# Kernel tuning notes

Measured on AMD Instinct MI355X. Metric: run time of the kernel, lower is better.

The kernel has to match this reference:

```python
import jax, jax.numpy as jnp
import numpy as np

B, N, C = 8, 6000, 21            # batch, proposals (pre_nms_topn), total_labels
VARIANCES = jnp.array([0.1, 0.1, 0.2, 0.2], jnp.float32)
MAX_TOTAL = 200                   # max_total_size == max_output_size_per_class
SCORE_THR = 0.5
IOU_THR = 0.5                     # tf combined_non_max_suppression default
NEG = -1e9                        # finite sentinel for suppressed scores


def setup_inputs() -> dict:
    key = jax.random.key(0)
    k1, k2, k3, k4 = jax.random.split(key, 4)
    # valid normalized rois: y1,x1 in [0,0.8), positive height/width
    yx1 = jax.random.uniform(k1, (B, N, 2), jnp.float32) * 0.8
    hw = jax.random.uniform(k4, (B, N, 2), jnp.float32) * 0.2 + 0.01
    roi_bboxes = jnp.concatenate([yx1, yx1 + hw], axis=-1)  # [B,N,4] y1x1y2x2
    pred_deltas = jax.random.normal(k2, (B, N, C * 4), jnp.float32) * 0.5
    pred_label_probs = jax.random.uniform(k3, (B, N, C), jnp.float32)
    return {"roi_bboxes": roi_bboxes, "pred_deltas": pred_deltas,
            "pred_label_probs": pred_label_probs}


def reference(roi_bboxes, pred_deltas, pred_label_probs):
    # --- bbox delta decoding ---
    deltas = pred_deltas.reshape(B, N, C, 4) * VARIANCES          # [B,N,C,4]
    roi = roi_bboxes[:, :, None, :]                               # [B,N,1,4]
    anc_h = roi[..., 2] - roi[..., 0]
    anc_w = roi[..., 3] - roi[..., 1]
    anc_cy = roi[..., 0] + 0.5 * anc_h
    anc_cx = roi[..., 1] + 0.5 * anc_w
    bh = jnp.exp(deltas[..., 2]) * anc_h
    bw = jnp.exp(deltas[..., 3]) * anc_w
    bcy = deltas[..., 0] * anc_h + anc_cy
    bcx = deltas[..., 1] * anc_w + anc_cx
    y1 = bcy - 0.5 * bh
    x1 = bcx - 0.5 * bw
    y2 = y1 + bh
    x2 = x1 + bw
    boxes = jnp.stack([y1, x1, y2, x2], axis=-1)                  # [B,N,C,4]
    boxes = jnp.clip(boxes, 0.0, 1.0)  # combined NMS clip_boxes=True default

    # zero out scores where argmax class is background (0)
    lbl = jnp.argmax(pred_label_probs, axis=-1)                   # [B,N]
    scores = jnp.where((lbl != 0)[..., None], pred_label_probs, 0.0)

    boxes = boxes.transpose(0, 2, 1, 3)                           # [B,C,N,4]
    scores = scores.transpose(0, 2, 1)                            # [B,C,N]
    s0 = jnp.where(scores > SCORE_THR, scores, NEG)

    areas = (jnp.maximum(boxes[..., 2] - boxes[..., 0], 0.0) *
             jnp.maximum(boxes[..., 3] - boxes[..., 1], 0.0))     # [B,C,N]

    # --- greedy per-class NMS, vectorized over (B,C) ---
    def step(s, _):
        idx = jnp.argmax(s, axis=-1)                              # [B,C]
        val = jnp.take_along_axis(s, idx[..., None], axis=-1)[..., 0]
        box = jnp.take_along_axis(boxes, idx[..., None, None], axis=2)[..., 0, :]
        valid = val > NEG * 0.5
        iy1 = jnp.maximum(box[..., None, 0], boxes[..., 0])
        ix1 = jnp.maximum(box[..., None, 1], boxes[..., 1])
        iy2 = jnp.minimum(box[..., None, 2], boxes[..., 2])
        ix2 = jnp.minimum(box[..., None, 3], boxes[..., 3])
        inter = jnp.maximum(iy2 - iy1, 0.0) * jnp.maximum(ix2 - ix1, 0.0)
        sel_a = (jnp.maximum(box[..., 2] - box[..., 0], 0.0) *
                 jnp.maximum(box[..., 3] - box[..., 1], 0.0))
        iou = inter / (sel_a[..., None] + areas - inter + 1e-8)   # [B,C,N]
        s = jnp.where((iou > IOU_THR) & valid[..., None], NEG, s)
        return s, (box, val, valid)

    _, (sel_box, sel_val, sel_ok) = jax.lax.scan(step, s0, None, length=MAX_TOTAL)
    # [T,B,C,*] -> [B, C*T, *]
    sel_box = sel_box.transpose(1, 2, 0, 3).reshape(B, C * MAX_TOTAL, 4)
    sel_val = sel_val.transpose(1, 2, 0).reshape(B, C * MAX_TOTAL)
    sel_ok = sel_ok.transpose(1, 2, 0).reshape(B, C * MAX_TOTAL)
    cls = jnp.broadcast_to(jnp.arange(C, dtype=jnp.float32)[None, :, None],
                           (B, C, MAX_TOTAL)).reshape(B, C * MAX_TOTAL)

    sel_val = jnp.where(sel_ok, sel_val, NEG)
    top_s, top_i = jax.lax.top_k(sel_val, MAX_TOTAL)              # [B,200]
    fb = jnp.take_along_axis(sel_box, top_i[..., None], axis=1)
    fc = jnp.take_along_axis(cls, top_i, axis=1)
    ok = top_s > NEG * 0.5
    final_scores = jnp.where(ok, top_s, 0.0)
    final_bboxes = jnp.where(ok[..., None], fb, 0.0)
    final_labels = jnp.where(ok, fc, 0.0)
    return final_bboxes, final_labels, final_scores
```

## Files before the change

### kernel.cpp

```cpp
#include <hip/hip_runtime.h>

#define B_    8
#define N_    6000
#define C_    21
#define MAXT  200
#define NEGV  -1000000000.0f
#define UCAP  4096
#define CCAP  1024
#define CTGT  512
#define NBUCK 64
#define NTH   1024
#define NENT  (C_ * MAXT)
#define NBLK  (B_ * C_)


__device__ __forceinline__ unsigned ford(float f) {
  unsigned u = __float_as_uint(f);
  return (u & 0x80000000u) ? ~u : (u | 0x80000000u);
}
__device__ __forceinline__ float funord(unsigned o) {
  unsigned u = (o & 0x80000000u) ? (o ^ 0x80000000u) : ~o;
  return __uint_as_float(u);
}

__device__ __forceinline__ float4 decode_box(const float* __restrict__ roi,
                                             const float* __restrict__ deltas,
                                             int b, int n, int c)
{
#pragma clang fp contract(off)
  float4 r = *(const float4*)(roi + ((size_t)b * N_ + n) * 4);
  float4 d = *(const float4*)(deltas + ((size_t)b * N_ + n) * (C_ * 4) + c * 4);
  float d0 = d.x * 0.1f, d1 = d.y * 0.1f, d2 = d.z * 0.2f, d3 = d.w * 0.2f;
  float ah = r.z - r.x, aw = r.w - r.y;
  float acy = r.x + 0.5f * ah, acx = r.y + 0.5f * aw;
  float bh = expf(d2) * ah, bw = expf(d3) * aw;
  float bcy = d0 * ah + acy, bcx = d1 * aw + acx;
  float y1 = bcy - 0.5f * bh, x1 = bcx - 0.5f * bw;
  float y2 = y1 + bh, x2 = x1 + bw;
  y1 = fminf(fmaxf(y1, 0.f), 1.f); x1 = fminf(fmaxf(x1, 0.f), 1.f);
  y2 = fminf(fmaxf(y2, 0.f), 1.f); x2 = fminf(fmaxf(x2, 0.f), 1.f);
  return make_float4(y1, x1, y2, x2);
}

__device__ __forceinline__ float iou_ref(float4 s, float4 o) {
#pragma clang fp contract(off)
  float iy1 = fmaxf(s.x, o.x), ix1 = fmaxf(s.y, o.y);
  float iy2 = fminf(s.z, o.z), ix2 = fminf(s.w, o.w);
  float inter = fmaxf(iy2 - iy1, 0.f) * fmaxf(ix2 - ix1, 0.f);
  float sa = fmaxf(s.z - s.x, 0.f) * fmaxf(s.w - s.y, 0.f);
  float oa = fmaxf(o.z - o.x, 0.f) * fmaxf(o.w - o.y, 0.f);
  return inter / (sa + oa - inter + 1e-08f);
}

struct Smem {
  unsigned long long ukeys[UCAP];
  unsigned long long cbuf[CCAP];
  float4 cboxAll[512];
  float4 comm[MAXT];
  unsigned long long kill[64];
  unsigned long long s_dead[16];
  int hist[NBUCK];
  int ctr[NBUCK];
  int wcnt[16];
  int s_cnt, s_clen, s_ncomm, s_blo, s_len, s_m, s_mx;
};

__global__ __launch_bounds__(256) void prep_kernel(
    const float* __restrict__ probs, float* __restrict__ probsT)
{
  int t = blockIdx.x * 256 + threadIdx.x;
  if (t >= B_ * N_) return;
  int b = t / N_, n = t - b * N_;
  const float* pr = probs + (size_t)t * C_;
  float p[C_];
  #pragma unroll
  for (int k = 0; k < C_; ++k) p[k] = pr[k];
  float mx = p[0]; int am = 0;
  #pragma unroll
  for (int k = 1; k < C_; ++k) { if (p[k] > mx) { mx = p[k]; am = k; } }
  float msk = (am != 0) ? 1.0f : 0.0f;
  #pragma unroll
  for (int c = 0; c < C_; ++c)
    probsT[((size_t)b * C_ + c) * N_ + n] = p[c] * msk;
}

__global__ __launch_bounds__(NTH) void nms_kernel(
    const float* __restrict__ roi, const float* __restrict__ deltas,
    const float* __restrict__ probs, const float* __restrict__ probsT,
    float* __restrict__ sel_val, float* __restrict__ sel_box)
{
#pragma clang fp contract(off)
  __shared__ Smem sm;
  const int bc = blockIdx.x, b = bc / C_, c = bc % C_;
  const int tid = threadIdx.x, lane = tid & 63, wv = tid >> 6;

  if (tid < NBUCK) sm.hist[tid] = 0;
  if (tid == 0) { sm.s_cnt = 0; sm.s_ncomm = 0; }
  __syncthreads();

  int M;
  const float* rowT = probsT ? (probsT + (size_t)bc * N_) : nullptr;
  if (rowT) {
    float scv[6];
    #pragma unroll
    for (int it = 0; it < 6; ++it) {
      int n = it * NTH + tid;
      scv[it] = (n < N_) ? rowT[n] : 0.f;
    }
    int off[6];
    int wtot = 0;
    #pragma unroll
    for (int it = 0; it < 6; ++it) {
      bool cand = (scv[it] > 0.5f);
      unsigned long long m = __ballot(cand);
      off[it] = wtot + __popcll(m & ((1ULL << lane) - 1ULL));
      wtot += __popcll(m);
    }
    if (lane == 0) sm.wcnt[wv] = wtot;
    __syncthreads();
    int wbase = 0, mtot = 0;
    #pragma unroll
    for (int w = 0; w < 16; ++w) {
      int t2 = sm.wcnt[w];
      if (w < wv) wbase += t2;
      mtot += t2;
    }
    #pragma unroll
    for (int it = 0; it < 6; ++it) {
      if (scv[it] > 0.5f) {
        int pos = wbase + off[it];
        if (pos < UCAP) {
          unsigned hi = ford(scv[it]);
          int n = it * NTH + tid;
          sm.ukeys[pos] = ((unsigned long long)hi << 32) |
                          (unsigned)(0xFFFFFFFFu - (unsigned)n);
          atomicAdd(&sm.hist[(hi >> 17) & (NBUCK - 1)], 1);
        }
      }
    }
    __syncthreads();
    M = mtot < UCAP ? mtot : UCAP;
  } else {
    for (int base0 = 0; base0 < N_; base0 += NTH) {
      int n = base0 + tid;
      bool cand = false;
      float sc = 0.f;
      if (n < N_) {
        const float* pr = probs + ((size_t)b * N_ + n) * C_;
        float mx = pr[0]; int am = 0;
        #pragma unroll
        for (int k = 1; k < C_; ++k) { float v = pr[k]; if (v > mx) { mx = v; am = k; } }
        if (am != 0) sc = pr[c];
        cand = (sc > 0.5f);
      }
      unsigned long long m = __ballot(cand);
      int wcnt2 = __popcll(m);
      int bslot = 0;
      if (lane == 0 && wcnt2) bslot = atomicAdd(&sm.s_cnt, wcnt2);
      bslot = __shfl(bslot, 0);
      if (cand) {
        int pos = bslot + __popcll(m & ((1ULL << lane) - 1ULL));
        if (pos < UCAP) {
          unsigned hi = ford(sc);
          sm.ukeys[pos] = ((unsigned long long)hi << 32) |
                          (unsigned)(0xFFFFFFFFu - (unsigned)n);
          atomicAdd(&sm.hist[(hi >> 17) & (NBUCK - 1)], 1);
        }
      }
    }
    __syncthreads();
    M = sm.s_cnt < UCAP ? sm.s_cnt : UCAP;
  }

  float* sv = sel_val + (size_t)bc * MAXT;
  float* sb = sel_box + (size_t)bc * MAXT * 4;

  int bhi = NBUCK - 1;
  while (true) {
    if (sm.s_ncomm >= MAXT || bhi < 0) break;

    if (wv == 0) {
      int h = (lane <= bhi) ? sm.hist[bhi - lane] : 0;
      int p = h;
      #pragma unroll
      for (int d = 1; d < 64; d <<= 1) {
        int o = __shfl_up(p, d);
        if (lane >= d) p += o;
      }
      unsigned long long ok = __ballot(p <= CTGT);
      int m = __popcll(ok);
      if (m == 0) m = 1;
      if (m > bhi + 1) m = bhi + 1;
      int len = __shfl(p, m - 1);
      if (lane < m) sm.ctr[bhi - lane] = p - h;
      int hv = (lane < m) ? h : 0;
      #pragma unroll
      for (int d = 1; d < 64; d <<= 1) hv = max(hv, __shfl_xor(hv, d));
      if (lane == 0) {
        sm.s_blo = bhi - (m - 1); sm.s_len = len; sm.s_clen = 0;
        sm.s_m = m; sm.s_mx = hv;
      }
    }
    __syncthreads();
    int blo = sm.s_blo;
    if (sm.s_len == 0) break;
    int mbk = sm.s_m, mxb = sm.s_mx;

    for (int i = tid; i < M; i += NTH) {
      unsigned long long kk = sm.ukeys[i];
      int bk = (int)((kk >> 49) & (NBUCK - 1));
      if (bk >= blo && bk <= bhi) {
        int slot = atomicAdd(&sm.ctr[bk], 1);
        if (slot < CCAP) sm.cbuf[slot] = kk;
      }
    }
    __syncthreads();
    int alen = sm.s_len < CCAP ? sm.s_len : CCAP;

    if (alen > 0) {
      if (alen <= 512 && mxb <= 128) {
        for (int j = wv; j < mbk; j += 16) {
          int bk = bhi - j;
          int len = sm.hist[bk];
          if (len <= 0) continue;
          int base = sm.ctr[bk] - len;
          if (len <= 64) {
            unsigned long long v = (lane < len) ? sm.cbuf[base + lane] : 0ULL;
            #pragma unroll
            for (int k = 2; k <= 64; k <<= 1) {
              for (int jj = k >> 1; jj > 0; jj >>= 1) {
                unsigned long long w = __shfl_xor(v, jj);
                bool takeMax = ((lane & jj) == 0) == ((lane & k) == 0);
                if ((w > v) == takeMax) v = w;
              }
            }
            if (lane < len) sm.cbuf[base + lane] = v;
          } else {
            unsigned long long v0 = (lane < len) ? sm.cbuf[base + lane] : 0ULL;
            unsigned long long v1 = (64 + lane < len) ? sm.cbuf[base + 64 + lane] : 0ULL;
            #pragma unroll
            for (int k = 2; k <= 128; k <<= 1) {
              for (int jj = k >> 1; jj > 0; jj >>= 1) {
                if (jj == 64) {
                  unsigned long long a = (v0 > v1) ? v0 : v1;
                  unsigned long long bmin = (v0 > v1) ? v1 : v0;
                  v0 = a; v1 = bmin;
                } else {
                  unsigned long long w0 = __shfl_xor(v0, jj);
                  unsigned long long w1 = __shfl_xor(v1, jj);
                  bool e0k = ((lane & k) == 0);
                  bool e1k = (((lane + 64) & k) == 0);
                  bool jz = ((lane & jj) == 0);
                  bool tm0 = (jz == e0k);
                  bool tm1 = (jz == e1k);
                  if ((w0 > v0) == tm0) v0 = w0;
                  if ((w1 > v1) == tm1) v1 = w1;
                }
              }
            }
            if (lane < len) sm.cbuf[base + lane] = v0;
            if (64 + lane < len) sm.cbuf[base + 64 + lane] = v1;
          }
        }
        __syncthreads();
      } else {
        int SORTP = 64;
        while (SORTP < alen) SORTP <<= 1;
        unsigned long long v = (tid < alen) ? sm.cbuf[tid] : 0ULL;
        for (int k = 2; k <= SORTP; k <<= 1) {
          for (int j = k >> 1; j > 0; j >>= 1) {
            bool takeMax = ((tid & j) == 0) == ((tid & k) == 0);
            unsigned long long w;
            if (j >= 64) {
              __syncthreads(); if (tid < SORTP) sm.cbuf[tid] = v; __syncthreads();
              w = sm.cbuf[tid ^ j];
            } else {
              w = __shfl_xor(v, j);
            }
            if (tid < SORTP && (w > v) == takeMax) v = w;
          }
        }
        __syncthreads();
        if (tid < SORTP) sm.cbuf[tid] = v;
        __syncthreads();
      }

      if (tid < alen && tid < 512) {
        int n = (int)(0xFFFFFFFFu - (unsigned)(sm.cbuf[tid] & 0xFFFFFFFFull));
        sm.cboxAll[tid] = decode_box(roi, deltas, b, n, c);
      }
      __syncthreads();

      int start = 0;
      int wlen = alen < 512 ? alen : 512;
      while (true) {
        int nc = sm.s_ncomm;
        if (nc >= MAXT || start >= wlen) break;
        int bs = min(64, wlen - start);

        float4 ib = sm.cboxAll[start + lane];
        #pragma unroll
        for (int r = 0; r < 4; ++r) {
          int j = (wv << 2) | r;
          float4 jb4 = sm.cboxAll[start + j];
          bool kf = (j < bs) && (lane < bs) && (lane > j) &&
                    (iou_ref(jb4, ib) > 0.5f);
          unsigned long long rowm = __ballot(kf);
          if (lane == 0) sm.kill[j] = rowm;
        }
        {
          bool dead = false;
          if (lane < bs) {
            for (int jc = wv; jc < nc; jc += 16) {
              if (iou_ref(sm.comm[jc], ib) > 0.5f) { dead = true; break; }
            }
          }
          unsigned long long dm = __ballot(dead);
          if (lane == 0) sm.s_dead[wv] = dm;
        }
        __syncthreads();

        if (wv == 0) {
          unsigned long long sup = sm.s_dead[0];
          #pragma unroll
          for (int w2 = 1; w2 < 16; ++w2) sup |= sm.s_dead[w2];
          unsigned long long row = sm.kill[lane];
          #pragma unroll
          for (int s5 = 0; s5 < 6; ++s5) {
            const unsigned long long Ms[6] = {
              0x5555555555555555ULL, 0x3333333333333333ULL,
              0x0F0F0F0F0F0F0F0FULL, 0x00FF00FF00FF00FFULL,
              0x0000FFFF0000FFFFULL, 0x00000000FFFFFFFFULL };
            int d = 1 << s5;
            unsigned long long other = __shfl_xor(row, d);
            unsigned long long Mk = Ms[s5];
            row = ((lane & d) == 0) ? ((row & Mk) | ((other & Mk) << d))
                                    : ((row & ~Mk) | ((other & ~Mk) >> d));
          }
          unsigned long long col = row;

          unsigned long long alive = ~sup;
          if (bs < 64) alive &= (1ULL << bs) - 1ULL;
          unsigned long long pend = alive, chosen = 0ULL;
          while (pend) {
            bool rdy_b = ((col & pend) == 0ULL);
            unsigned long long rdy = __ballot(rdy_b) & pend;
            bool kld_b = ((col & chosen) != 0ULL);
            unsigned long long kl = __ballot(kld_b);
            chosen |= rdy & ~kl;
            pend &= ~rdy;
          }
          int take = MAXT - nc;
          if (__popcll(chosen) > take) {
            bool keep = ((chosen >> lane) & 1ULL) &&
                        (__popcll(chosen & ((1ULL << lane) - 1ULL)) < take);
            chosen = __ballot(keep);
          }
          if ((chosen >> lane) & 1ULL) {
            int rnk = nc + __popcll(chosen & ((1ULL << lane) - 1ULL));
            float4 bb2 = sm.cboxAll[start + lane];
            sm.comm[rnk] = bb2;
            sv[rnk] = funord((unsigned)(sm.cbuf[start + lane] >> 32));
            sb[(size_t)rnk * 4 + 0] = bb2.x; sb[(size_t)rnk * 4 + 1] = bb2.y;
            sb[(size_t)rnk * 4 + 2] = bb2.z; sb[(size_t)rnk * 4 + 3] = bb2.w;
          }
          if (lane == 0) sm.s_ncomm = nc + __popcll(chosen);
        }
        __syncthreads();
        start += bs;
      }
    }
    bhi = blo - 1;
  }

  int T = sm.s_ncomm;
  for (int j2 = T + tid; j2 < MAXT; j2 += NTH) sv[j2] = NEGV;
}

__global__ __launch_bounds__(NTH) void merge2_kernel(
    const float* __restrict__ sel_val, const float* __restrict__ sel_box,
    float* __restrict__ out)
{
  __shared__ Smem sm;
  const int bc = blockIdx.x;
  const int b = bc / C_, sc = bc % C_;
  const int tid = threadIdx.x;
  int* s_rank = reinterpret_cast<int*>(sm.cboxAll);

  for (int i = tid; i < NENT; i += NTH) {
    float v = sel_val[(size_t)b * NENT + i];
    unsigned long long key = ((unsigned long long)ford(v) << 32) |
                             (unsigned)(0xFFFFFFFFu - (unsigned)i);
    if (i < UCAP) sm.ukeys[i] = key; else sm.cbuf[i - UCAP] = key;
  }
  if (tid < MAXT) s_rank[tid] = 0;
  __syncthreads();

  auto klds = [&](int i) -> unsigned long long {
    return (i < UCAP) ? sm.ukeys[i] : sm.cbuf[i - UCAP];
  };

  if (tid < 1000) {
    int q = tid / MAXT, t = tid - q * MAXT;
    int e = sc * MAXT + t;
    unsigned long long mykey = klds(e);
    int part = 0;
    for (int cc = q; cc < C_; cc += 5) {
      int lo = 0, hi = MAXT;
      while (lo < hi) {
        int mid = (lo + hi) >> 1;
        if (klds(cc * MAXT + mid) > mykey) lo = mid + 1; else hi = mid;
      }
      part += lo;
    }
    atomicAdd(&s_rank[t], part);
  }
  __syncthreads();

  if (tid < MAXT) {
    int t = tid;
    int e = sc * MAXT + t;
    int rank = s_rank[t];
    if (rank < MAXT) {
      float* obx = out + (size_t)b * MAXT * 4;
      float* olb = out + (size_t)B_ * MAXT * 4 + (size_t)b * MAXT;
      float* osc = out + (size_t)B_ * MAXT * 5 + (size_t)b * MAXT;
      float v = funord((unsigned)(klds(e) >> 32));
      if (v > NEGV * 0.5f) {
        osc[rank] = v;
        olb[rank] = (float)sc;
        const float* bp = sel_box + ((size_t)b * NENT + e) * 4;
        obx[rank * 4 + 0] = bp[0]; obx[rank * 4 + 1] = bp[1];
        obx[rank * 4 + 2] = bp[2]; obx[rank * 4 + 3] = bp[3];
      } else {
        osc[rank] = 0.f; olb[rank] = 0.f;
        obx[rank * 4 + 0] = 0.f; obx[rank * 4 + 1] = 0.f;
        obx[rank * 4 + 2] = 0.f; obx[rank * 4 + 3] = 0.f;
      }
    }
  }
}

extern "C" void kernel_launch(void* const* d_in, const int* in_sizes, int n_in,
                              void* d_out, int out_size, void* d_ws, size_t ws_size,
                              hipStream_t stream)
{
  const float* roi    = (const float*)d_in[0];
  const float* deltas = (const float*)d_in[1];
  const float* probs  = (const float*)d_in[2];
  float* out = (float*)d_out;
  float* ws  = (float*)d_ws;

  float* sel_val = ws;
  float* sel_box = ws + (size_t)B_ * NENT;
  float* probsT  = ws + (size_t)B_ * NENT * 5;
  size_t need_mid = ((size_t)B_ * NENT * 5 + (size_t)B_ * C_ * N_) * sizeof(float);
  bool haveT = (ws_size >= need_mid);

  const float* probsT_arg = haveT ? probsT : nullptr;
  if (haveT)
    prep_kernel<<<dim3((B_ * N_ + 255) / 256), dim3(256), 0, stream>>>(probs, probsT);
  nms_kernel<<<dim3(NBLK), dim3(NTH), 0, stream>>>(
      roi, deltas, probs, probsT_arg, sel_val, sel_box);
  merge2_kernel<<<dim3(NBLK), dim3(NTH), 0, stream>>>(sel_val, sel_box, out);
}
```

Measured before the change: 97.51 us.

## Fuse merge into NMS kernel via per-batch atomic counter barrier

Folds the merge step into the end of the NMS kernel. The C_ blocks of each batch wait on a global atomic counter that prep_kernel resets, and once all have arrived they run the rank-and-scatter merge in place. This removes one kernel launch and the gap between launches. It depends on all 168 blocks of 1024 threads being resident at the same time, otherwise the spin-wait could deadlock. The separate merge kernel is kept as a fallback when the workspace is too small.

```diff
diff --git a/kernel.cpp b/kernel.cpp
--- a/kernel.cpp
+++ b/kernel.cpp
@@ -65,10 +65,73 @@
   int s_cnt, s_clen, s_ncomm, s_blo, s_len, s_m, s_mx;
 };
 
+__device__ void merge_body(const float* __restrict__ sel_val,
+                           const float* __restrict__ sel_box,
+                           float* __restrict__ out,
+                           int b, int sc, Smem& sm, int tid)
+{
+  int* s_rank = reinterpret_cast<int*>(sm.cboxAll);
+
+  for (int i = tid; i < NENT; i += NTH) {
+    float v = sel_val[(size_t)b * NENT + i];
+    unsigned long long key = ((unsigned long long)ford(v) << 32) |
+                             (unsigned)(0xFFFFFFFFu - (unsigned)i);
+    if (i < UCAP) sm.ukeys[i] = key; else sm.cbuf[i - UCAP] = key;
+  }
+  if (tid < MAXT) s_rank[tid] = 0;
+  __syncthreads();
+
+  auto klds = [&](int i) -> unsigned long long {
+    return (i < UCAP) ? sm.ukeys[i] : sm.cbuf[i - UCAP];
+  };
+
+  if (tid < 1000) {
+    int q = tid / MAXT, t = tid - q * MAXT;
+    int e = sc * MAXT + t;
+    unsigned long long mykey = klds(e);
+    int part = 0;
+    for (int cc = q; cc < C_; cc += 5) {
+      int lo = 0, hi = MAXT;
+      while (lo < hi) {
+        int mid = (lo + hi) >> 1;
+        if (klds(cc * MAXT + mid) > mykey) lo = mid + 1; else hi = mid;
+      }
+      part += lo;
+    }
+    atomicAdd(&s_rank[t], part);
+  }
+  __syncthreads();
+
+  if (tid < MAXT) {
+    int t = tid;
+    int e = sc * MAXT + t;
+    int rank = s_rank[t];
+    if (rank < MAXT) {
+      float* obx = out + (size_t)b * MAXT * 4;
+      float* olb = out + (size_t)B_ * MAXT * 4 + (size_t)b * MAXT;
+      float* osc = out + (size_t)B_ * MAXT * 5 + (size_t)b * MAXT;
+      float v = funord((unsigned)(klds(e) >> 32));
+      if (v > NEGV * 0.5f) {
+        osc[rank] = v;
+        olb[rank] = (float)sc;
+        const float* bp = sel_box + ((size_t)b * NENT + e) * 4;
+        obx[rank * 4 + 0] = bp[0]; obx[rank * 4 + 1] = bp[1];
+        obx[rank * 4 + 2] = bp[2]; obx[rank * 4 + 3] = bp[3];
+      } else {
+        osc[rank] = 0.f; olb[rank] = 0.f;
+        obx[rank * 4 + 0] = 0.f; obx[rank * 4 + 1] = 0.f;
+        obx[rank * 4 + 2] = 0.f; obx[rank * 4 + 3] = 0.f;
+      }
+    }
+  }
+}
+
 __global__ __launch_bounds__(256) void prep_kernel(
-    const float* __restrict__ probs, float* __restrict__ probsT)
+    const float* __restrict__ probs, float* __restrict__ probsT,
+    int* __restrict__ bcnt)
 {
   int t = blockIdx.x * 256 + threadIdx.x;
+  if (blockIdx.x == 0 && threadIdx.x < B_) bcnt[threadIdx.x] = 0;
   if (t >= B_ * N_) return;
   int b = t / N_, n = t - b * N_;
   const float* pr = probs + (size_t)t * C_;
@@ -87,7 +150,8 @@
 __global__ __launch_bounds__(NTH) void nms_kernel(
     const float* __restrict__ roi, const float* __restrict__ deltas,
     const float* __restrict__ probs, const float* __restrict__ probsT,
-    float* __restrict__ sel_val, float* __restrict__ sel_box)
+    float* __restrict__ sel_val, float* __restrict__ sel_box,
+    float* __restrict__ out, int* __restrict__ bcnt)
 {
 #pragma clang fp contract(off)
   __shared__ Smem sm;
@@ -375,6 +439,20 @@
 
   int T = sm.s_ncomm;
   for (int j2 = T + tid; j2 < MAXT; j2 += NTH) sv[j2] = NEGV;
+
+  if (bcnt != nullptr) {
+    __syncthreads();
+    if (tid == 0) {
+      __threadfence();
+      atomicAdd(&bcnt[b], 1);
+      while (__hip_atomic_load(&bcnt[b], __ATOMIC_RELAXED,
+                               __HIP_MEMORY_SCOPE_AGENT) < C_)
+        __builtin_amdgcn_s_sleep(8);
+      __threadfence();
+    }
+    __syncthreads();
+    merge_body(sel_val, sel_box, out, b, c, sm, tid);
+  }
 }
 
 __global__ __launch_bounds__(NTH) void merge2_kernel(
@@ -383,62 +461,7 @@
 {
   __shared__ Smem sm;
   const int bc = blockIdx.x;
-  const int b = bc / C_, sc = bc % C_;
-  const int tid = threadIdx.x;
-  int* s_rank = reinterpret_cast<int*>(sm.cboxAll);
-
-  for (int i = tid; i < NENT; i += NTH) {
-    float v = sel_val[(size_t)b * NENT + i];
-    unsigned long long key = ((unsigned long long)ford(v) << 32) |
-                             (unsigned)(0xFFFFFFFFu - (unsigned)i);
-    if (i < UCAP) sm.ukeys[i] = key; else sm.cbuf[i - UCAP] = key;
-  }
-  if (tid < MAXT) s_rank[tid] = 0;
-  __syncthreads();
-
-  auto klds = [&](int i) -> unsigned long long {
-    return (i < UCAP) ? sm.ukeys[i] : sm.cbuf[i - UCAP];
-  };
-
-  if (tid < 1000) {
-    int q = tid / MAXT, t = tid - q * MAXT;
-    int e = sc * MAXT + t;
-    unsigned long long mykey = klds(e);
-    int part = 0;
-    for (int cc = q; cc < C_; cc += 5) {
-      int lo = 0, hi = MAXT;
-      while (lo < hi) {
-        int mid = (lo + hi) >> 1;
-        if (klds(cc * MAXT + mid) > mykey) lo = mid + 1; else hi = mid;
-      }
-      part += lo;
-    }
-    atomicAdd(&s_rank[t], part);
-  }
-  __syncthreads();
-
-  if (tid < MAXT) {
-    int t = tid;
-    int e = sc * MAXT + t;
-    int rank = s_rank[t];
-    if (rank < MAXT) {
-      float* obx = out + (size_t)b * MAXT * 4;
-      float* olb = out + (size_t)B_ * MAXT * 4 + (size_t)b * MAXT;
-      float* osc = out + (size_t)B_ * MAXT * 5 + (size_t)b * MAXT;
-      float v = funord((unsigned)(klds(e) >> 32));
-      if (v > NEGV * 0.5f) {
-        osc[rank] = v;
-        olb[rank] = (float)sc;
-        const float* bp = sel_box + ((size_t)b * NENT + e) * 4;
-        obx[rank * 4 + 0] = bp[0]; obx[rank * 4 + 1] = bp[1];
-        obx[rank * 4 + 2] = bp[2]; obx[rank * 4 + 3] = bp[3];
-      } else {
-        osc[rank] = 0.f; olb[rank] = 0.f;
-        obx[rank * 4 + 0] = 0.f; obx[rank * 4 + 1] = 0.f;
-        obx[rank * 4 + 2] = 0.f; obx[rank * 4 + 3] = 0.f;
-      }
-    }
-  }
+  merge_body(sel_val, sel_box, out, bc / C_, bc % C_, sm, threadIdx.x);
 }
 
 extern "C" void kernel_launch(void* const* d_in, const int* in_sizes, int n_in,
@@ -454,13 +477,19 @@
   float* sel_val = ws;
   float* sel_box = ws + (size_t)B_ * NENT;
   float* probsT  = ws + (size_t)B_ * NENT * 5;
-  size_t need_mid = ((size_t)B_ * NENT * 5 + (size_t)B_ * C_ * N_) * sizeof(float);
+  int*   bcnt    = (int*)(ws + (size_t)B_ * NENT * 5 + (size_t)B_ * C_ * N_);
+  size_t need_mid = ((size_t)B_ * NENT * 5 + (size_t)B_ * C_ * N_) * sizeof(float)
+                  + B_ * sizeof(int);
   bool haveT = (ws_size >= need_mid);
 
-  const float* probsT_arg = haveT ? probsT : nullptr;
-  if (haveT)
-    prep_kernel<<<dim3((B_ * N_ + 255) / 256), dim3(256), 0, stream>>>(probs, probsT);
-  nms_kernel<<<dim3(NBLK), dim3(NTH), 0, stream>>>(
-      roi, deltas, probs, probsT_arg, sel_val, sel_box);
-  merge2_kernel<<<dim3(NBLK), dim3(NTH), 0, stream>>>(sel_val, sel_box, out);
-}
+  if (haveT) {
+    prep_kernel<<<dim3((B_ * N_ + 255) / 256), dim3(256), 0, stream>>>(
+        probs, probsT, bcnt);
+    nms_kernel<<<dim3(NBLK), dim3(NTH), 0, stream>>>(
+        roi, deltas, probs, probsT, sel_val, sel_box, out, bcnt);
+  } else {
+    nms_kernel<<<dim3(NBLK), dim3(NTH), 0, stream>>>(
+        roi, deltas, probs, nullptr, sel_val, sel_box, out, nullptr);
+    merge2_kernel<<<dim3(NBLK), dim3(NTH), 0, stream>>>(sel_val, sel_box, out);
+  }
+}
```

Result: slower. 105.2 us (+7.9%).
